# Kernel optimization log

Measured on AMD Instinct MI355X. Metric: run time of the kernel, lower is better.

Reference implementation:

```python
import jax, jax.numpy as jnp
import numpy as np

N_QUBITS = 14
N_LAYERS = 3
BATCH = 128


def _apply_1q(state, gate, w, n):
    """Apply a single-qubit gate on wire w (PennyLane wire 0 = most significant bit).
    state: (B, 2**n) complex. gate: (2,2) shared or (B,2,2) batched."""
    L, R = 2 ** w, 2 ** (n - 1 - w)
    s = state.reshape(-1, L, 2, R)
    if gate.ndim == 2:
        s = jnp.einsum('ij,aljr->alir', gate, s)
    else:
        s = jnp.einsum('aij,aljr->alir', gate, s)
    return s.reshape(state.shape)


def _apply_cnot(state, c, t, n):
    """CNOT with control wire c, target wire t on (B, 2**n) state."""
    s = state.reshape((-1,) + (2,) * n)
    ca = 1 + c
    s0 = jax.lax.index_in_dim(s, 0, ca, keepdims=False)
    s1 = jax.lax.index_in_dim(s, 1, ca, keepdims=False)
    # axis of target after removing control axis
    ta = 1 + t if t < c else t
    s1 = jnp.flip(s1, axis=ta)
    return jnp.stack([s0, s1], axis=ca).reshape(state.shape)


def _rx_gates(angles):
    """Batched RX gate matrices. angles: (B,) -> (B,2,2) complex64."""
    half = angles * 0.5
    c = jnp.cos(half).astype(jnp.complex64)
    s = (-1j) * jnp.sin(half).astype(jnp.complex64)
    return jnp.stack([jnp.stack([c, s], -1), jnp.stack([s, c], -1)], -2)


def _rot_gate(phi, theta, omega):
    """PennyLane Rot(phi,theta,omega) = RZ(omega) RY(theta) RZ(phi), (2,2) complex."""
    ct = jnp.cos(theta * 0.5).astype(jnp.complex64)
    st = jnp.sin(theta * 0.5).astype(jnp.complex64)
    ep = jnp.exp(-0.5j * (phi + omega))  # e^{-i(phi+omega)/2}
    em = jnp.exp(-0.5j * (phi - omega))  # e^{-i(phi-omega)/2}
    return jnp.stack([
        jnp.stack([ep * ct, -jnp.conj(em) * st]),
        jnp.stack([em * st, jnp.conj(ep) * ct]),
    ]).astype(jnp.complex64)


def _simulate(x, q_weights):
    B, n = x.shape
    state = jnp.zeros((B, 2 ** n), jnp.complex64).at[:, 0].set(1.0)
    # AngleEmbedding: RX(x_i) on wire i
    for w in range(n):
        state = _apply_1q(state, _rx_gates(x[:, w]), w, n)
    # StronglyEntanglingLayers: Rot on each wire, then ring of CNOTs with range r
    n_layers = q_weights.shape[0]
    for l in range(n_layers):
        for w in range(n):
            g = _rot_gate(q_weights[l, w, 0], q_weights[l, w, 1], q_weights[l, w, 2])
            state = _apply_1q(state, g, w, n)
        r = (l % (n - 1)) + 1  # PennyLane default ranges
        for w in range(n):
            state = _apply_cnot(state, w, (w + r) % n, n)
    return state


def _pauli_z_signs(n):
    idx = np.arange(2 ** n, dtype=np.int64)[:, None]
    shifts = np.arange(n - 1, -1, -1, dtype=np.int64)[None, :]  # wire 0 = MSB
    bits = (idx >> shifts) & 1
    return jnp.asarray(1.0 - 2.0 * bits, dtype=jnp.float32)  # (2**n, n)


def setup_inputs() -> dict:
    key = jax.random.key(0)
    k1, k2, k3, k4 = jax.random.split(key, 4)
    x = jax.random.normal(k1, (BATCH, N_QUBITS), dtype=jnp.float32)
    q_weights = jax.random.normal(k2, (N_LAYERS, N_QUBITS, 3), dtype=jnp.float32) * 0.01
    w_lin = jax.random.normal(k3, (1, N_QUBITS), dtype=jnp.float32) / np.sqrt(N_QUBITS)
    b_lin = jax.random.normal(k4, (1,), dtype=jnp.float32) * 0.01
    return {"x": x, "q_weights": q_weights, "w_lin": w_lin, "b_lin": b_lin}


def reference(x, q_weights, w_lin, b_lin):
    n = x.shape[1]
    state = _simulate(x, q_weights)
    probs = (state.real ** 2 + state.imag ** 2).astype(jnp.float32)  # (B, 2**n)
    expvals = probs @ _pauli_z_signs(n)  # (B, n) = <Z_i>
    logits = expvals @ w_lin.T + b_lin  # (B, 1)
    return logits
```

## Files before the change

### kernel.cpp

```cpp
#include <hip/hip_runtime.h>

#define NQ 14
#define NSTATE (1 << NQ)
#define NL 3
#define NPASS (NL * 4)
#define BT 1024
#define NWAVES (BT / 64)

struct PassP {
    unsigned short R[10];
    unsigned short cmb[16];
    unsigned char gidx[4];
    unsigned char nw;
    unsigned char _pad;
};
struct SimParams {
    PassP pass[NPASS];
    unsigned short ms[NQ];
};

struct C2x2 { float2 m[2][2]; };

__device__ __forceinline__ float2 cmul(float2 a, float2 b) {
    return make_float2(a.x * b.x - a.y * b.y, a.x * b.y + a.y * b.x);
}
__device__ __forceinline__ float2 cmac(float2 acc, float2 a, float2 b) {
    acc.x = fmaf(a.x, b.x, fmaf(-a.y, b.y, acc.x));
    acc.y = fmaf(a.x, b.y, fmaf(a.y, b.x, acc.y));
    return acc;
}

__device__ __forceinline__ C2x2 rot_gate(const float* qp) {
    float phi = qp[0], th = qp[1], om = qp[2];
    float ct, stt; __sincosf(0.5f * th, &stt, &ct);
    float sa, ca; __sincosf(0.5f * (phi + om), &sa, &ca);
    float sb, cb; __sincosf(0.5f * (phi - om), &sb, &cb);
    C2x2 G;
    G.m[0][0] = make_float2(ca * ct, -sa * ct);
    G.m[0][1] = make_float2(-cb * stt, -sb * stt);
    G.m[1][0] = make_float2(cb * stt, -sb * stt);
    G.m[1][1] = make_float2(ca * ct, sa * ct);
    return G;
}

__device__ __forceinline__ C2x2 fuse_rx(C2x2 G, float ang) {
    float sh, ch; __sincosf(0.5f * ang, &sh, &ch);
    float2 c = make_float2(ch, 0.f), is = make_float2(0.f, -sh);
    C2x2 R;
    #pragma unroll
    for (int i = 0; i < 2; ++i) {
        R.m[i][0] = cmac(cmul(G.m[i][0], c), G.m[i][1], is);
        R.m[i][1] = cmac(cmul(G.m[i][1], c), G.m[i][0], is);
    }
    return R;
}

__global__ __launch_bounds__(BT) void qsim_kernel(
    const float* __restrict__ x, const float* __restrict__ qw,
    const float* __restrict__ wl, const float* __restrict__ bl,
    float* __restrict__ out, SimParams P)
{
    __shared__ float2 st[NSTATE];
    __shared__ float2 gbuf[NL * NQ * 4];
    __shared__ float red[NWAVES];

    const int tid = threadIdx.x;
    const int b = blockIdx.x;

    for (int t = tid; t < NSTATE; t += BT) st[t] = make_float2(0.f, 0.f);
    if (tid == 0) st[0] = make_float2(1.f, 0.f);

    if (tid < NL * NQ) {
        int l = tid / NQ, w = tid % NQ;
        C2x2 G = rot_gate(qw + tid * 3);
        if (l == 0) G = fuse_rx(G, x[b * NQ + w]);
        gbuf[tid * 4 + 0] = G.m[0][0];
        gbuf[tid * 4 + 1] = G.m[0][1];
        gbuf[tid * 4 + 2] = G.m[1][0];
        gbuf[tid * 4 + 3] = G.m[1][1];
    }

    #pragma unroll 1
    for (int ps = 0; ps < NPASS; ++ps) {
        __syncthreads();

        unsigned r = 0;
        #pragma unroll
        for (int j = 0; j < 10; ++j)
            r ^= ((tid >> j) & 1) ? (unsigned)P.pass[ps].R[j] : 0u;
        const unsigned rb = r << 3;

        unsigned c8[16];
        #pragma unroll
        for (int i = 0; i < 16; ++i)
            c8[i] = ((unsigned)P.pass[ps].cmb[i]) << 3;

        char* sb = (char*)st;
        float2 a[16];
        #pragma unroll
        for (int i = 0; i < 16; ++i)
            a[i] = *(const float2*)(sb + (rb ^ c8[i]));

        const int nw = P.pass[ps].nw;
        #pragma unroll
        for (int q = 0; q < 4; ++q) {
            if (q < nw) {
                const int gi = (int)P.pass[ps].gidx[q] * 4;
                float2 g00 = gbuf[gi + 0], g01 = gbuf[gi + 1];
                float2 g10 = gbuf[gi + 2], g11 = gbuf[gi + 3];
                #pragma unroll
                for (int i = 0; i < 16; ++i) {
                    if (!((i >> q) & 1)) {
                        const int i1 = i | (1 << q);
                        float2 a0 = a[i], a1 = a[i1];
                        float2 n0 = cmac(cmul(g00, a0), g01, a1);
                        float2 n1 = cmac(cmul(g10, a0), g11, a1);
                        a[i] = n0; a[i1] = n1;
                    }
                }
            }
        }

        #pragma unroll
        for (int i = 0; i < 16; ++i)
            *(float2*)(sb + (rb ^ c8[i])) = a[i];
    }

    __syncthreads();

    float A[16];
    #pragma unroll
    for (int k = 0; k < 16; ++k) A[k] = 0.f;
    #pragma unroll
    for (int w = 0; w < NQ; ++w) {
        const unsigned msw = (unsigned)P.ms[w];
        float v = wl[w];
        unsigned s0 = __popc((unsigned)tid & (msw & 1023u)) & 1u;
        float vs = s0 ? -v : v;
        const unsigned hk = msw >> 10;
        #pragma unroll
        for (int k = 0; k < 16; ++k) {
            bool neg = (__popc((unsigned)k & hk) & 1) != 0;
            A[k] += neg ? -vs : vs;
        }
    }

    float acc = 0.f;
    #pragma unroll
    for (int k = 0; k < 16; ++k) {
        float2 a = st[k * BT + tid];
        acc = fmaf(fmaf(a.x, a.x, a.y * a.y), A[k], acc);
    }

    #pragma unroll
    for (int off = 32; off > 0; off >>= 1) acc += __shfl_down(acc, off, 64);
    int lane = tid & 63, wid = tid >> 6;
    if (lane == 0) red[wid] = acc;
    __syncthreads();
    if (tid == 0) {
        float s = 0.f;
        #pragma unroll
        for (int i = 0; i < NWAVES; ++i) s += red[i];
        out[b] = s + bl[0];
    }
}

struct GF2Basis {
    unsigned piv[NQ];
    GF2Basis() { for (int i = 0; i < NQ; ++i) piv[i] = 0; }
    bool insert(unsigned v) {
        for (int bb = NQ - 1; bb >= 0; --bb) {
            if (!((v >> bb) & 1)) continue;
            if (piv[bb]) v ^= piv[bb];
            else { piv[bb] = v; return true; }
        }
        return false;
    }
};

static inline int par16(unsigned v) { return __builtin_parity(v); }
static inline unsigned lcg_next(unsigned& s) { s = s * 1664525u + 1013904223u; return s >> 8; }

static unsigned gf_apply(const unsigned* C, unsigned v) {
    unsigned r = 0;
    while (v) { int j = __builtin_ctz(v); v &= v - 1; r ^= C[j]; }
    return r;
}

static bool gf_invert(const unsigned* C, unsigned* Ci) {
    unsigned rows[NQ], irows[NQ];
    for (int i = 0; i < NQ; ++i) {
        unsigned r = 0;
        for (int j = 0; j < NQ; ++j) r |= ((C[j] >> i) & 1u) << j;
        rows[i] = r; irows[i] = 1u << i;
    }
    for (int c = 0; c < NQ; ++c) {
        int p = -1;
        for (int r = c; r < NQ; ++r) if ((rows[r] >> c) & 1u) { p = r; break; }
        if (p < 0) return false;
        unsigned t = rows[p]; rows[p] = rows[c]; rows[c] = t;
        t = irows[p]; irows[p] = irows[c]; irows[c] = t;
        for (int r = 0; r < NQ; ++r)
            if (r != c && ((rows[r] >> c) & 1u)) { rows[r] ^= rows[c]; irows[r] ^= irows[c]; }
    }
    for (int j = 0; j < NQ; ++j) {
        unsigned col = 0;
        for (int i = 0; i < NQ; ++i) col |= ((irows[i] >> j) & 1u) << i;
        Ci[j] = col;
    }
    return true;
}

extern "C" void kernel_launch(void* const* d_in, const int* in_sizes, int n_in,
                              void* d_out, int out_size, void* d_ws, size_t ws_size,
                              hipStream_t stream) {
    const float* x  = (const float*)d_in[0];
    const float* qw = (const float*)d_in[1];
    const float* wl = (const float*)d_in[2];
    const float* bl = (const float*)d_in[3];
    float* out = (float*)d_out;

    const int B = in_sizes[0] / NQ;

    struct Raw { unsigned mm[4], rv[10], cmb[16]; unsigned char gidx[4], nw; } raw[NPASS];
    unsigned s[NQ], m[NQ], msIdx[NQ];
    for (int w = 0; w < NQ; ++w) s[w] = m[w] = 1u << (NQ - 1 - w);

    int ps = 0;
    for (int l = 0; l < NL; ++l) {
        for (int g0 = 0; g0 < NQ; g0 += 4) {
            int nw = (NQ - g0) < 4 ? (NQ - g0) : 4;
            unsigned mm[4], ss[4];
            GF2Basis gf;
            for (int i = 0; i < nw; ++i) { mm[i] = m[g0 + i]; ss[i] = s[g0 + i]; gf.insert(mm[i]); }
            for (int i = nw; i < 4; ++i) {
                unsigned cand = 0;
                for (int t = 0; t < NQ; ++t)
                    if (gf.insert(1u << t)) { cand = 1u << t; break; }
                for (int j = 0; j < nw; ++j)
                    if (par16(cand & ss[j])) cand ^= mm[j];
                mm[i] = cand; ss[i] = 0;
            }
            int nR = 0;
            for (int t = 0; t < NQ && nR < 10; ++t) {
                if (gf.insert(1u << t)) {
                    unsigned v = 1u << t;
                    for (int j = 0; j < nw; ++j)
                        if (par16(v & ss[j])) v ^= mm[j];
                    raw[ps].rv[nR++] = v;
                }
            }
            for (int idx = 0; idx < 16; ++idx) {
                unsigned c = 0;
                for (int q = 0; q < 4; ++q) if ((idx >> q) & 1) c ^= mm[q];
                raw[ps].cmb[idx] = c;
                if (idx < 4) raw[ps].mm[idx] = mm[idx];
            }
            for (int q = 0; q < 4; ++q)
                raw[ps].gidx[q] = (unsigned char)(q < nw ? (l * NQ + g0 + q) : 0);
            raw[ps].nw = (unsigned char)nw;
            ++ps;
        }
        int r = (l % (NQ - 1)) + 1;
        for (int w = 0; w < NQ; ++w) {
            int c = w, t = (w + r) % NQ;
            s[t] ^= s[c];
            m[c] ^= m[t];
        }
    }
    for (int w = 0; w < NQ; ++w) msIdx[w] = s[w];

    unsigned Cm[NQ], Ci[NQ];
    unsigned seed = 0x9E3779B9u;
    bool found = false;
    for (int tries = 0; tries < 5000 && !found; ++tries) {
        for (int j = 0; j < NQ; ++j) Cm[j] = lcg_next(seed) & (NSTATE - 1);
        if (!gf_invert(Cm, Ci)) continue;
        found = true;
        for (int p = 0; p < NPASS && found; ++p) {
            unsigned piv[4] = {0, 0, 0, 0}; int np = 0;
            for (int i = 0; i < 10; ++i) {
                unsigned w2 = gf_apply(Cm, raw[p].rv[i]);
                for (int bb = 0; bb < 4; ++bb)
                    if (((w2 >> bb) & 1u) && piv[bb]) w2 ^= piv[bb];
                if ((w2 & 15u) && np < 4) { piv[__builtin_ctz(w2 & 15u)] = w2; ++np; }
            }
            if (np < 4) found = false;
        }
    }
    if (!found) {
        for (int j = 0; j < NQ; ++j) Cm[j] = 1u << j;
        gf_invert(Cm, Ci);
    }

    SimParams P;
    for (int p = 0; p < NPASS; ++p) {
        unsigned u[10];
        for (int i = 0; i < 10; ++i) u[i] = gf_apply(Cm, raw[p].rv[i]);
        unsigned piv[4] = {0, 0, 0, 0};
        int ord[10], np = 0, rest[10], nrest = 0;
        for (int i = 0; i < 10; ++i) {
            unsigned w2 = u[i];
            for (int bb = 0; bb < 4; ++bb)
                if (((w2 >> bb) & 1u) && piv[bb]) w2 ^= piv[bb];
            if ((w2 & 15u) && np < 4) { piv[__builtin_ctz(w2 & 15u)] = w2; ord[np++] = i; }
            else rest[nrest++] = i;
        }
        int kk = 0;
        for (int i = 0; i < np; ++i) P.pass[p].R[kk++] = (unsigned short)u[ord[i]];
        for (int i = 0; i < nrest; ++i) P.pass[p].R[kk++] = (unsigned short)u[rest[i]];
        for (int idx = 0; idx < 16; ++idx)
            P.pass[p].cmb[idx] = (unsigned short)gf_apply(Cm, raw[p].cmb[idx]);
        for (int q = 0; q < 4; ++q) P.pass[p].gidx[q] = raw[p].gidx[q];
        P.pass[p].nw = raw[p].nw;
        P.pass[p]._pad = 0;
    }
    for (int w = 0; w < NQ; ++w) {
        unsigned msp = 0;
        for (int i = 0; i < NQ; ++i)
            msp |= (unsigned)(par16(Ci[i] & msIdx[w]) & 1) << i;
        P.ms[w] = (unsigned short)msp;
    }

    qsim_kernel<<<dim3(B), dim3(BT), 0, stream>>>(x, qw, wl, bl, out, P);
}
```

Before: 114.1 us.

## Greedily pack commuting gates into fewer passes and fuse init/readout into passes

The host now schedules gates greedily out of program order, packing up to four mutually commuting, linearly independent gates per pass, which can reduce the pass count below twelve. The kernel drops the separate shared-memory zeroing by having the first pass write a register-built initial state. It computes the Pauli-Z readout directly from registers in the final pass, avoiding an extra barrier and reread. It also precomputes the next pass's row offset. The commutation-based reordering must respect gate dependencies exactly, so a subtle ordering mistake would give wrong results.

```diff
diff --git a/kernel.cpp b/kernel.cpp
--- a/kernel.cpp
+++ b/kernel.cpp
@@ -3,7 +3,7 @@
 #define NQ 14
 #define NSTATE (1 << NQ)
 #define NL 3
-#define NPASS (NL * 4)
+#define MAXP 12
 #define BT 1024
 #define NWAVES (BT / 64)
 
@@ -15,8 +15,10 @@
     unsigned char _pad;
 };
 struct SimParams {
-    PassP pass[NPASS];
+    PassP pass[MAXP];
     unsigned short ms[NQ];
+    unsigned short fmask[NQ];
+    int np;
 };
 
 struct C2x2 { float2 m[2][2]; };
@@ -55,6 +57,29 @@
     return R;
 }
 
+#define APPLY_STAGES(PSIDX)                                                 \
+    {                                                                       \
+        const int nw_ = P.pass[PSIDX].nw;                                   \
+        _Pragma("unroll")                                                   \
+        for (int q = 0; q < 4; ++q) {                                       \
+            if (q < nw_) {                         \
+                const int gi = (int)P.pass[PSIDX].gidx[q] * 4;              \
+                float2 g00 = gbuf[gi + 0], g01 = gbuf[gi + 1];              \
+                float2 g10 = gbuf[gi + 2], g11 = gbuf[gi + 3];              \
+                _Pragma("unroll")                                           \
+                for (int i = 0; i < 16; ++i) {                              \
+                    if (!((i >> q) & 1)) {                                  \
+                        const int i1 = i | (1 << q);                        \
+                        float2 a0 = a[i], a1 = a[i1];                       \
+                        float2 n0 = cmac(cmul(g00, a0), g01, a1);           \
+                        float2 n1 = cmac(cmul(g10, a0), g11, a1);           \
+                        a[i] = n0; a[i1] = n1;                              \
+                    }                                                       \
+                }                                                           \
+            }                                                               \
+        }                                                                   \
+    }
+
 __global__ __launch_bounds__(BT) void qsim_kernel(
     const float* __restrict__ x, const float* __restrict__ qw,
     const float* __restrict__ wl, const float* __restrict__ bl,
@@ -67,9 +92,6 @@
     const int tid = threadIdx.x;
     const int b = blockIdx.x;
 
-    for (int t = tid; t < NSTATE; t += BT) st[t] = make_float2(0.f, 0.f);
-    if (tid == 0) st[0] = make_float2(1.f, 0.f);
-
     if (tid < NL * NQ) {
         int l = tid / NQ, w = tid % NQ;
         C2x2 G = rot_gate(qw + tid * 3);
@@ -80,88 +102,100 @@
         gbuf[tid * 4 + 3] = G.m[1][1];
     }
 
+    const int np = P.np;
+    char* sb = (char*)st;
+    float2 a[16];
+    unsigned addr[16];
+
+    unsigned r0 = 0;
+    #pragma unroll
+    for (int j = 0; j < 10; ++j)
+        r0 ^= ((tid >> j) & 1) ? (unsigned)P.pass[0].R[j] : 0u;
+
+    __syncthreads();
+
+    {
+        const unsigned rb = r0 << 3;
+        #pragma unroll
+        for (int i = 0; i < 16; ++i)
+            addr[i] = rb ^ (((unsigned)P.pass[0].cmb[i]) << 3);
+        #pragma unroll
+        for (int i = 0; i < 16; ++i) a[i] = make_float2(0.f, 0.f);
+        if (tid == 0) {
+            a[0] = make_float2(1.f, 0.f);
+            APPLY_STAGES(0);
+        }
+        #pragma unroll
+        for (int i = 0; i < 16; ++i)
+            *(float2*)(sb + addr[i]) = a[i];
+    }
+
+    unsigned rn = 0;
+    #pragma unroll
+    for (int j = 0; j < 10; ++j)
+        rn ^= ((tid >> j) & 1) ? (unsigned)P.pass[1].R[j] : 0u;
+
     #pragma unroll 1
-    for (int ps = 0; ps < NPASS; ++ps) {
+    for (int ps = 1; ps < np - 1; ++ps) {
         __syncthreads();
-
-        unsigned r = 0;
+        const unsigned rb = rn << 3;
+        #pragma unroll
+        for (int i = 0; i < 16; ++i)
+            addr[i] = rb ^ (((unsigned)P.pass[ps].cmb[i]) << 3);
+        #pragma unroll
+        for (int i = 0; i < 16; ++i)
+            a[i] = *(const float2*)(sb + addr[i]);
+        unsigned rt = 0;
         #pragma unroll
         for (int j = 0; j < 10; ++j)
-            r ^= ((tid >> j) & 1) ? (unsigned)P.pass[ps].R[j] : 0u;
-        const unsigned rb = r << 3;
-
-        unsigned c8[16];
-        #pragma unroll
-        for (int i = 0; i < 16; ++i)
-            c8[i] = ((unsigned)P.pass[ps].cmb[i]) << 3;
-
-        char* sb = (char*)st;
-        float2 a[16];
-        #pragma unroll
-        for (int i = 0; i < 16; ++i)
-            a[i] = *(const float2*)(sb + (rb ^ c8[i]));
-
-        const int nw = P.pass[ps].nw;
-        #pragma unroll
-        for (int q = 0; q < 4; ++q) {
-            if (q < nw) {
-                const int gi = (int)P.pass[ps].gidx[q] * 4;
-                float2 g00 = gbuf[gi + 0], g01 = gbuf[gi + 1];
-                float2 g10 = gbuf[gi + 2], g11 = gbuf[gi + 3];
-                #pragma unroll
-                for (int i = 0; i < 16; ++i) {
-                    if (!((i >> q) & 1)) {
-                        const int i1 = i | (1 << q);
-                        float2 a0 = a[i], a1 = a[i1];
-                        float2 n0 = cmac(cmul(g00, a0), g01, a1);
-                        float2 n1 = cmac(cmul(g10, a0), g11, a1);
-                        a[i] = n0; a[i1] = n1;
-                    }
-                }
-            }
-        }
-
-        #pragma unroll
-        for (int i = 0; i < 16; ++i)
-            *(float2*)(sb + (rb ^ c8[i])) = a[i];
-    }
-
-    __syncthreads();
-
-    float A[16];
-    #pragma unroll
-    for (int k = 0; k < 16; ++k) A[k] = 0.f;
-    #pragma unroll
-    for (int w = 0; w < NQ; ++w) {
-        const unsigned msw = (unsigned)P.ms[w];
-        float v = wl[w];
-        unsigned s0 = __popc((unsigned)tid & (msw & 1023u)) & 1u;
-        float vs = s0 ? -v : v;
-        const unsigned hk = msw >> 10;
-        #pragma unroll
-        for (int k = 0; k < 16; ++k) {
-            bool neg = (__popc((unsigned)k & hk) & 1) != 0;
-            A[k] += neg ? -vs : vs;
-        }
+            rt ^= ((tid >> j) & 1) ? (unsigned)P.pass[ps + 1].R[j] : 0u;
+        APPLY_STAGES(ps);
+        rn = rt;
+        #pragma unroll
+        for (int i = 0; i < 16; ++i)
+            *(float2*)(sb + addr[i]) = a[i];
     }
 
     float acc = 0.f;
-    #pragma unroll
-    for (int k = 0; k < 16; ++k) {
-        float2 a = st[k * BT + tid];
-        acc = fmaf(fmaf(a.x, a.x, a.y * a.y), A[k], acc);
+    {
+        const int ps = np - 1;
+        __syncthreads();
+        const unsigned rb = rn << 3;
+        #pragma unroll
+        for (int i = 0; i < 16; ++i)
+            addr[i] = rb ^ (((unsigned)P.pass[ps].cmb[i]) << 3);
+        #pragma unroll
+        for (int i = 0; i < 16; ++i)
+            a[i] = *(const float2*)(sb + addr[i]);
+        APPLY_STAGES(ps);
+
+        float A[16];
+        #pragma unroll
+        for (int i = 0; i < 16; ++i) A[i] = 0.f;
+        #pragma unroll
+        for (int w = 0; w < NQ; ++w) {
+            float v = wl[w];
+            unsigned p0 = __popc(rn & (unsigned)P.ms[w]) & 1u;
+            float vs = p0 ? -v : v;
+            const unsigned fm = (unsigned)P.fmask[w];
+            #pragma unroll
+            for (int i = 0; i < 16; ++i)
+                A[i] += ((fm >> i) & 1u) ? -vs : vs;
+        }
+        #pragma unroll
+        for (int i = 0; i < 16; ++i)
+            acc = fmaf(fmaf(a[i].x, a[i].x, a[i].y * a[i].y), A[i], acc);
     }
 
     #pragma unroll
     for (int off = 32; off > 0; off >>= 1) acc += __shfl_down(acc, off, 64);
-    int lane = tid & 63, wid = tid >> 6;
-    if (lane == 0) red[wid] = acc;
+    if ((tid & 63) == 0) red[tid >> 6] = acc;
     __syncthreads();
     if (tid == 0) {
-        float s = 0.f;
-        #pragma unroll
-        for (int i = 0; i < NWAVES; ++i) s += red[i];
-        out[b] = s + bl[0];
+        float s2 = 0.f;
+        #pragma unroll
+        for (int i = 0; i < NWAVES; ++i) s2 += red[i];
+        out[b] = s2 + bl[0];
     }
 }
 
@@ -222,44 +256,14 @@
 
     const int B = in_sizes[0] / NQ;
 
-    struct Raw { unsigned mm[4], rv[10], cmb[16]; unsigned char gidx[4], nw; } raw[NPASS];
+    unsigned gs[NL * NQ], gm[NL * NQ];
+    int ggi[NL * NQ];
     unsigned s[NQ], m[NQ], msIdx[NQ];
     for (int w = 0; w < NQ; ++w) s[w] = m[w] = 1u << (NQ - 1 - w);
-
-    int ps = 0;
+    int ng = 0;
     for (int l = 0; l < NL; ++l) {
-        for (int g0 = 0; g0 < NQ; g0 += 4) {
-            int nw = (NQ - g0) < 4 ? (NQ - g0) : 4;
-            unsigned mm[4], ss[4];
-            GF2Basis gf;
-            for (int i = 0; i < nw; ++i) { mm[i] = m[g0 + i]; ss[i] = s[g0 + i]; gf.insert(mm[i]); }
-            for (int i = nw; i < 4; ++i) {
-                unsigned cand = 0;
-                for (int t = 0; t < NQ; ++t)
-                    if (gf.insert(1u << t)) { cand = 1u << t; break; }
-                for (int j = 0; j < nw; ++j)
-                    if (par16(cand & ss[j])) cand ^= mm[j];
-                mm[i] = cand; ss[i] = 0;
-            }
-            int nR = 0;
-            for (int t = 0; t < NQ && nR < 10; ++t) {
-                if (gf.insert(1u << t)) {
-                    unsigned v = 1u << t;
-                    for (int j = 0; j < nw; ++j)
-                        if (par16(v & ss[j])) v ^= mm[j];
-                    raw[ps].rv[nR++] = v;
-                }
-            }
-            for (int idx = 0; idx < 16; ++idx) {
-                unsigned c = 0;
-                for (int q = 0; q < 4; ++q) if ((idx >> q) & 1) c ^= mm[q];
-                raw[ps].cmb[idx] = c;
-                if (idx < 4) raw[ps].mm[idx] = mm[idx];
-            }
-            for (int q = 0; q < 4; ++q)
-                raw[ps].gidx[q] = (unsigned char)(q < nw ? (l * NQ + g0 + q) : 0);
-            raw[ps].nw = (unsigned char)nw;
-            ++ps;
+        for (int w = 0; w < NQ; ++w) {
+            gs[ng] = s[w]; gm[ng] = m[w]; ggi[ng] = l * NQ + w; ++ng;
         }
         int r = (l % (NQ - 1)) + 1;
         for (int w = 0; w < NQ; ++w) {
@@ -269,6 +273,57 @@
         }
     }
     for (int w = 0; w < NQ; ++w) msIdx[w] = s[w];
+
+    struct Raw { unsigned rv[10], cmb[16]; unsigned char gidx[4], nw; } raw[MAXP];
+    bool used[NL * NQ] = {false};
+    int np = 0, remaining = ng;
+    while (remaining > 0 && np < MAXP) {
+        unsigned pss[4], pmm[4];
+        int pgi[4], nw = 0;
+        GF2Basis gf;
+        for (int g = 0; g < ng && nw < 4; ++g) {
+            if (used[g]) continue;
+            bool ok = true;
+            for (int k = 0; k < nw && ok; ++k)
+                if (par16(gs[g] & pmm[k]) || par16(pss[k] & gm[g])) ok = false;
+            for (int h = 0; h < g && ok; ++h)
+                if (!used[h] && (par16(gs[g] & gm[h]) || par16(gs[h] & gm[g]))) ok = false;
+            if (!ok) continue;
+            GF2Basis trial = gf;
+            if (!trial.insert(gm[g])) continue;
+            gf = trial;
+            pss[nw] = gs[g]; pmm[nw] = gm[g]; pgi[nw] = g; ++nw;
+            used[g] = true; --remaining;
+        }
+        unsigned mm[4], ss[4];
+        for (int i = 0; i < nw; ++i) { mm[i] = pmm[i]; ss[i] = pss[i]; }
+        for (int i = nw; i < 4; ++i) {
+            unsigned cand = 0;
+            for (int t = 0; t < NQ; ++t)
+                if (gf.insert(1u << t)) { cand = 1u << t; break; }
+            for (int j = 0; j < nw; ++j)
+                if (par16(cand & ss[j])) cand ^= mm[j];
+            mm[i] = cand; ss[i] = 0;
+        }
+        int nR = 0;
+        for (int t = 0; t < NQ && nR < 10; ++t) {
+            if (gf.insert(1u << t)) {
+                unsigned v = 1u << t;
+                for (int j = 0; j < nw; ++j)
+                    if (par16(v & ss[j])) v ^= mm[j];
+                raw[np].rv[nR++] = v;
+            }
+        }
+        for (int idx = 0; idx < 16; ++idx) {
+            unsigned c = 0;
+            for (int q = 0; q < 4; ++q) if ((idx >> q) & 1) c ^= mm[q];
+            raw[np].cmb[idx] = c;
+        }
+        for (int q = 0; q < 4; ++q)
+            raw[np].gidx[q] = (unsigned char)(q < nw ? ggi[pgi[q]] : 0);
+        raw[np].nw = (unsigned char)nw;
+        ++np;
+    }
 
     unsigned Cm[NQ], Ci[NQ];
     unsigned seed = 0x9E3779B9u;
@@ -277,15 +332,15 @@
         for (int j = 0; j < NQ; ++j) Cm[j] = lcg_next(seed) & (NSTATE - 1);
         if (!gf_invert(Cm, Ci)) continue;
         found = true;
-        for (int p = 0; p < NPASS && found; ++p) {
-            unsigned piv[4] = {0, 0, 0, 0}; int np = 0;
+        for (int p = 0; p < np && found; ++p) {
+            unsigned piv[4] = {0, 0, 0, 0}; int npv = 0;
             for (int i = 0; i < 10; ++i) {
                 unsigned w2 = gf_apply(Cm, raw[p].rv[i]);
                 for (int bb = 0; bb < 4; ++bb)
                     if (((w2 >> bb) & 1u) && piv[bb]) w2 ^= piv[bb];
-                if ((w2 & 15u) && np < 4) { piv[__builtin_ctz(w2 & 15u)] = w2; ++np; }
+                if ((w2 & 15u) && npv < 4) { piv[__builtin_ctz(w2 & 15u)] = w2; ++npv; }
             }
-            if (np < 4) found = false;
+            if (npv < 4) found = false;
         }
     }
     if (!found) {
@@ -293,21 +348,22 @@
         gf_invert(Cm, Ci);
     }
 
-    SimParams P;
-    for (int p = 0; p < NPASS; ++p) {
+    SimParams P = {};
+    P.np = np;
+    for (int p = 0; p < np; ++p) {
         unsigned u[10];
         for (int i = 0; i < 10; ++i) u[i] = gf_apply(Cm, raw[p].rv[i]);
         unsigned piv[4] = {0, 0, 0, 0};
-        int ord[10], np = 0, rest[10], nrest = 0;
+        int ord[10], npv = 0, rest[10], nrest = 0;
         for (int i = 0; i < 10; ++i) {
             unsigned w2 = u[i];
             for (int bb = 0; bb < 4; ++bb)
                 if (((w2 >> bb) & 1u) && piv[bb]) w2 ^= piv[bb];
-            if ((w2 & 15u) && np < 4) { piv[__builtin_ctz(w2 & 15u)] = w2; ord[np++] = i; }
+            if ((w2 & 15u) && npv < 4) { piv[__builtin_ctz(w2 & 15u)] = w2; ord[npv++] = i; }
             else rest[nrest++] = i;
         }
         int kk = 0;
-        for (int i = 0; i < np; ++i) P.pass[p].R[kk++] = (unsigned short)u[ord[i]];
+        for (int i = 0; i < npv; ++i) P.pass[p].R[kk++] = (unsigned short)u[ord[i]];
         for (int i = 0; i < nrest; ++i) P.pass[p].R[kk++] = (unsigned short)u[rest[i]];
         for (int idx = 0; idx < 16; ++idx)
             P.pass[p].cmb[idx] = (unsigned short)gf_apply(Cm, raw[p].cmb[idx]);
@@ -321,6 +377,12 @@
             msp |= (unsigned)(par16(Ci[i] & msIdx[w]) & 1) << i;
         P.ms[w] = (unsigned short)msp;
     }
+    for (int w = 0; w < NQ; ++w) {
+        unsigned fm = 0;
+        for (int i = 0; i < 16; ++i)
+            fm |= (unsigned)(par16((unsigned)P.pass[np - 1].cmb[i] & (unsigned)P.ms[w]) & 1) << i;
+        P.fmask[w] = (unsigned short)fm;
+    }
 
     qsim_kernel<<<dim3(B), dim3(BT), 0, stream>>>(x, qw, wl, bl, out, P);
 }
```

Measured after the change: 110.0 us. -3.6%, faster.
